# Kernel optimization log

Hardware: AMD Instinct MI355X
Metric: run time of the kernel (lower is better)

## Reference

```python
import jax, jax.numpy as jnp
import numpy as np

B, H, W = 2, 128, 128
MID = 64            # mid_channels
DG = 16             # deform_groups
MAX_RES = 10.0      # max_residue_magnitude
CIN_OFF = 3 * MID + 4   # 196: cat(extra_feat, flow_1, flow_2)
COFF = DG * 27          # 432: o1 + o2 + mask, each DG*9


def setup_inputs() -> dict:
    key = jax.random.key(0)
    ks = jax.random.split(key, 9)
    return {
        "extra_feat": jax.random.normal(ks[0], (B, 3 * MID, H, W), jnp.float32),
        "flow_1": jax.random.normal(ks[1], (B, 2, H, W), jnp.float32) * 2.0,
        "flow_2": jax.random.normal(ks[2], (B, 2, H, W), jnp.float32) * 2.0,
        "feat_prop": jax.random.normal(ks[3], (B, MID, H, W), jnp.float32),
        "feat_n2": jax.random.normal(ks[4], (B, MID, H, W), jnp.float32),
        "w_off": jax.random.normal(ks[5], (COFF, CIN_OFF, 3, 3), jnp.float32) * 0.02,
        "b_off": jax.random.normal(ks[6], (COFF,), jnp.float32) * 0.02,
        "dc_weight": jax.random.normal(ks[7], (MID, 2 * MID, 3, 3), jnp.float32) * 0.05,
        "dc_bias": jax.random.normal(ks[8], (MID,), jnp.float32) * 0.05,
    }


def _conv3x3(x, w, b):
    y = jax.lax.conv_general_dilated(
        x, w, window_strides=(1, 1), padding=((1, 1), (1, 1)),
        dimension_numbers=("NCHW", "OIHW", "NCHW"))
    return y + b[None, :, None, None]


def _deform_conv2d(inp, offset, mask, weight, bias):
    # inp: [B, Cin, H, W]; offset: [B, 2*DG*9, H, W] (per group, per kernel pos: (dy, dx));
    # mask: [B, DG*9, H, W]; weight: [Cout, Cin, 3, 3]; stride=1, pad=1, dil=1.
    Bb, Cin, Hi, Wi = inp.shape
    K = 9
    cg = Cin // DG
    Ho, Wo = Hi, Wi
    ki = jnp.repeat(jnp.arange(3), 3)  # kernel row index per flat k (row-major)
    kj = jnp.tile(jnp.arange(3), 3)
    base_y = (jnp.arange(Ho) - 1)[None, :, None] + ki[:, None, None]  # [K, Ho, 1]
    base_x = (jnp.arange(Wo) - 1)[None, None, :] + kj[:, None, None]  # [K, 1, Wo]
    off = offset.reshape(Bb, DG, K, 2, Ho, Wo)
    py = base_y[None, None] + off[:, :, :, 0]  # [B, DG, K, Ho, Wo]
    px = base_x[None, None] + off[:, :, :, 1]
    y0 = jnp.floor(py)
    x0 = jnp.floor(px)
    inp_g = inp.reshape(Bb, DG, cg, Hi * Wi)
    acc = jnp.zeros((Bb, DG, cg, K, Ho, Wo), inp.dtype)
    for dy in (0.0, 1.0):
        for dx in (0.0, 1.0):
            yc = y0 + dy
            xc = x0 + dx
            wgt = (1.0 - jnp.abs(py - yc)) * (1.0 - jnp.abs(px - xc))
            valid = (yc >= 0) & (yc < Hi) & (xc >= 0) & (xc < Wi)
            idx = (jnp.clip(yc, 0, Hi - 1) * Wi + jnp.clip(xc, 0, Wi - 1)).astype(jnp.int32)
            idx = jnp.broadcast_to(idx.reshape(Bb, DG, 1, K * Ho * Wo), (Bb, DG, cg, K * Ho * Wo))
            g = jnp.take_along_axis(inp_g, idx, axis=3).reshape(Bb, DG, cg, K, Ho, Wo)
            acc = acc + g * (wgt * valid)[:, :, None]
    sm = acc * mask.reshape(Bb, DG, 1, K, Ho, Wo)  # modulated samples
    wr = weight.reshape(weight.shape[0], DG, cg, K)
    out = jnp.einsum("bgckhw,ogck->bohw", sm, wr) + bias[None, :, None, None]
    return out


def reference(extra_feat, flow_1, flow_2, feat_prop, feat_n2, w_off, b_off, dc_weight, dc_bias):
    x = jnp.concatenate([extra_feat, flow_1, flow_2], axis=1)
    out = _conv3x3(x, w_off, b_off)
    o1, o2, m = jnp.split(out, 3, axis=1)  # each [B, DG*9, H, W]
    offset = MAX_RES * jnp.tanh(jnp.concatenate([o1, o2], axis=1))
    rep = DG * 3 * 3 // 2  # 72
    f1 = jnp.tile(flow_1[:, ::-1], (1, rep, 1, 1))  # flip(1): (dx,dy)->(dy,dx)
    f2 = jnp.tile(flow_2[:, ::-1], (1, rep, 1, 1))
    half = offset.shape[1] // 2
    offset = jnp.concatenate([offset[:, :half] + f1, offset[:, half:] + f2], axis=1)
    mask = jax.nn.sigmoid(m)
    inp = jnp.concatenate([feat_prop, feat_n2], axis=1)
    return _deform_conv2d(inp, offset, mask, dc_weight, dc_bias)
```

## Files before the change

### kernel.cpp

```cpp
#include <hip/hip_runtime.h>
#include <math.h>

#define Hh 128
#define Ww 128
#define HW (128*128)
#define CIN_OFF 196
#define COFF 432

typedef _Float16 half8 __attribute__((ext_vector_type(8)));
typedef _Float16 half4 __attribute__((ext_vector_type(4)));
typedef _Float16 half2v __attribute__((ext_vector_type(2)));
typedef float f32x4 __attribute__((ext_vector_type(4)));

static __device__ __forceinline__ half8 splat8(float v) {
  _Float16 h = (_Float16)v;
  half8 r = {h, h, h, h, h, h, h, h};
  return r;
}

__global__ __launch_bounds__(256) void k_prep_all(
    const float* __restrict__ dcw, const float* __restrict__ w_off,
    const float* __restrict__ fp, const float* __restrict__ fn2,
    _Float16* __restrict__ wH, _Float16* __restrict__ BpT, _Float16* __restrict__ Bt,
    _Float16* __restrict__ featT) {
  const int bid = blockIdx.x;
  if (bid < 3375) {
    const int idx = bid * 256 + (int)threadIdx.x;
    if (idx < 73728) {
      const int co = idx / 1152;
      const int j  = idx - co * 1152;
      const int k  = j >> 7;
      const int ci = j & 127;
      wH[idx] = (_Float16)dcw[(co * 128 + ci) * 9 + k];
    } else if (idx < 73728 + 774144) {
      const int j  = idx - 73728;
      const int c  = j & 7;
      const int n  = (j >> 3) % 448;
      const int sl = (j >> 3) / 448;
      const int l4 = sl & 3;
      const int s  = sl >> 2;
      const int t  = s / 6;
      const int cg = s - t * 6;
      const int ci = cg * 32 + l4 * 8 + c;
      BpT[j] = (_Float16)((n < COFF) ? w_off[((size_t)n * CIN_OFF + ci) * 9 + t] : 0.f);
    } else {
      const int j = idx - 73728 - 774144;
      const int c = j & 3;
      const int n = (j >> 2) % 448;
      const int t = (j >> 2) / 448;
      Bt[j] = (_Float16)((n < COFF) ? w_off[((size_t)n * CIN_OFF + 192 + c) * 9 + t] : 0.f);
    }
  } else {
    const int t = (bid - 3375) * 256 + (int)threadIdx.x;
    const int b = t >> 14;
    const int hw = t & 16383;
#pragma unroll
    for (int g = 0; g < 16; ++g) {
      const float* src = (g < 8) ? fp : fn2;
      const int ch0 = (g & 7) * 8;
      half8 v;
#pragma unroll
      for (int c = 0; c < 8; ++c)
        v[c] = (_Float16)src[(size_t)(b * 64 + ch0 + c) * HW + hw];
      *(half8*)(featT + (((size_t)(b * 16 + g)) * HW + hw) * 8) = v;
    }
  }
}

__global__ __launch_bounds__(512, 2) void k_offconv_mfma(
    const float* __restrict__ extra, const float* __restrict__ f1, const float* __restrict__ f2,
    const _Float16* __restrict__ BpT, const _Float16* __restrict__ Bt,
    const float* __restrict__ b_off,
    _Float16* __restrict__ off_pm, _Float16* __restrict__ mask_pm) {
  __shared__ __align__(16) _Float16 smA[3 * 130 * 192];
  __shared__ __align__(16) _Float16 smT[3 * 130 * 4];
  const int h    = blockIdx.x;
  const int b    = blockIdx.y;
  const int tid  = (int)threadIdx.x;
  const int lane = tid & 63;
  const int wid  = tid >> 6;
  const int wm   = wid & 1;
  const int wn   = (wid >> 1) & 3;
  const int m_base = wm * 64;
  const int n_base = wn * 112;
  const int l15 = lane & 15;
  const int l4  = lane >> 4;

  for (int z = tid; z < 588; z += 512) {
    const int p2 = z % 98;
    const int rr = z / 98;
    const int r  = (rr >= 3) ? (rr - 3) : rr;
    const int px = (rr >= 3) ? 129 : 0;
    if (p2 < 96) {
      const int ci = 2 * p2, biw = ci >> 3;
      const int sw = ((biw & 24) | ((biw & 7) ^ (px & 7))) << 3;
      *(half2v*)(smA + (r * 130 + px) * 192 + sw + (ci & 7)) = (half2v){(_Float16)0.f, (_Float16)0.f};
    } else {
      *(half2v*)(smT + (r * 130 + px) * 4 + 2 * (p2 - 96)) = (half2v){(_Float16)0.f, (_Float16)0.f};
    }
  }

#pragma unroll 3
  for (int j = 0; j < 18; ++j) {
    const int J   = tid + 512 * j;
    const int p2a = J & 15;
    const int qa  = (J >> 4) & 3;
    const int R   = J >> 6;
    const int r   = R / 48;
    const int rem = R - 48 * r;
    const int qh  = rem & 7;
    const int p2h = rem >> 3;
    const int q   = qa + 4 * qh;
    const int p2  = p2a + 16 * p2h;
    const int ci  = 2 * p2;
    const int gh  = h - 1 + r;
    float4 va = {0.f, 0.f, 0.f, 0.f}, vb = va;
    if ((unsigned)gh < (unsigned)Hh) {
      const float* xp = extra + (size_t)(b * 192 + ci) * HW + gh * Ww + 4 * q;
      va = *(const float4*)xp;
      vb = *(const float4*)(xp + HW);
    }
    const float av[4] = {va.x, va.y, va.z, va.w};
    const float bv[4] = {vb.x, vb.y, vb.z, vb.w};
    const int biw = p2 >> 2;
#pragma unroll
    for (int i = 0; i < 4; ++i) {
      const int px = 1 + 4 * q + i;
      const int sw = ((biw & 24) | ((biw & 7) ^ (px & 7))) << 3;
      half2v pk; pk[0] = (_Float16)av[i]; pk[1] = (_Float16)bv[i];
      *(half2v*)(smA + (r * 130 + px) * 192 + sw + (ci & 7)) = pk;
    }
  }
  if (tid < 192) {
    const int q   = tid & 31;
    const int p2t = (tid >> 5) & 1;
    const int r   = tid >> 6;
    const int gh  = h - 1 + r;
    float4 va = {0.f, 0.f, 0.f, 0.f}, vb = va;
    if ((unsigned)gh < (unsigned)Hh) {
      const float* xp = (p2t ? f2 : f1) + (size_t)(b * 2) * HW + gh * Ww + 4 * q;
      va = *(const float4*)xp;
      vb = *(const float4*)(xp + HW);
    }
    const float av[4] = {va.x, va.y, va.z, va.w};
    const float bv[4] = {vb.x, vb.y, vb.z, vb.w};
#pragma unroll
    for (int i = 0; i < 4; ++i) {
      const int px = 1 + 4 * q + i;
      half2v pk; pk[0] = (_Float16)av[i]; pk[1] = (_Float16)bv[i];
      *(half2v*)(smT + (r * 130 + px) * 4 + 2 * p2t) = pk;
    }
  }
  __syncthreads();

  f32x4 acc[4][7];
#pragma unroll
  for (int i = 0; i < 4; ++i)
#pragma unroll
    for (int j = 0; j < 7; ++j) acc[i][j] = (f32x4){0.f, 0.f, 0.f, 0.f};

  const bool lz = (l4 == 0);
#pragma unroll 3
  for (int t = 0; t < 9; ++t) {
    const int ki = t / 3;
    const int kj = t - 3 * ki;
#pragma unroll
    for (int cg = 0; cg < 6; ++cg) {
      const int s4 = ((t * 6 + cg) * 4 + l4) * 448;
      half8 bf[7];
#pragma unroll
      for (int f = 0; f < 7; ++f)
        bf[f] = *(const half8*)(BpT + (size_t)(s4 + n_base + f * 16 + l15) * 8);
      half8 af[4];
#pragma unroll
      for (int mf = 0; mf < 4; ++mf) {
        const int px = m_base + mf * 16 + l15 + kj;
        const int bi = cg * 4 + l4;
        af[mf] = *(const half8*)(smA + (ki * 130 + px) * 192 +
                                 (((bi & 24) | ((bi & 7) ^ (px & 7))) << 3));
      }
#pragma unroll
      for (int mf = 0; mf < 4; ++mf)
#pragma unroll
        for (int f = 0; f < 7; ++f)
          acc[mf][f] = __builtin_amdgcn_mfma_f32_16x16x32_f16(af[mf], bf[f], acc[mf][f], 0, 0, 0);
    }
    half8 aft[4];
#pragma unroll
    for (int mf = 0; mf < 4; ++mf) {
      const int px = m_base + mf * 16 + l15 + kj;
      const half4 tv = *(const half4*)(smT + (ki * 130 + px) * 4);
      half8 a = {0, 0, 0, 0, 0, 0, 0, 0};
      if (lz) { a[0] = tv[0]; a[1] = tv[1]; a[2] = tv[2]; a[3] = tv[3]; }
      aft[mf] = a;
    }
#pragma unroll
    for (int f = 0; f < 7; ++f) {
      const half4 wv = *(const half4*)(Bt + (size_t)(t * 448 + n_base + f * 16 + l15) * 4);
      half8 bb = {0, 0, 0, 0, 0, 0, 0, 0};
      if (lz) { bb[0] = wv[0]; bb[1] = wv[1]; bb[2] = wv[2]; bb[3] = wv[3]; }
#pragma unroll
      for (int mf = 0; mf < 4; ++mf)
        acc[mf][f] = __builtin_amdgcn_mfma_f32_16x16x32_f16(aft[mf], bb, acc[mf][f], 0, 0, 0);
    }
  }

  __syncthreads();
  _Float16* so = smA;
  const int hw0 = h * Ww;
#pragma unroll
  for (int f = 0; f < 7; ++f) {
    const int n = n_base + f * 16 + l15;
    const float bias = (n < COFF) ? b_off[n] : 0.f;
    const bool isOff = (n < 288);
    const float* fl = (n < 144) ? f1 : f2;
    const size_t fladd = (size_t)(b * 2 + ((n & 1) ^ 1)) * HW + hw0;
#pragma unroll
    for (int mf = 0; mf < 4; ++mf) {
#pragma unroll
      for (int rr = 0; rr < 4; ++rr) {
        const int px = m_base + mf * 16 + l4 * 4 + rr;
        const float v = acc[mf][f][rr] + bias;
        float val;
        if (isOff) {
          const float e = __expf(2.f * v);
          val = 10.f * (1.f - 2.f / (e + 1.f)) + fl[fladd + px];
        } else {
          val = 1.f / (1.f + __expf(-v));
        }
        so[px * 456 + n] = (_Float16)val;
      }
    }
  }
  __syncthreads();
  for (int T = tid; T < 4608; T += 512) {
    const int px = T / 36, c = T - px * 36;
    const half8 v = *(const half8*)(so + px * 456 + c * 8);
    *(half8*)(off_pm + ((size_t)b * HW + hw0 + px) * 288 + c * 8) = v;
  }
  for (int T = tid; T < 2304; T += 512) {
    const int px = T / 18, c = T - px * 18;
    const half8 v = *(const half8*)(so + px * 456 + 288 + c * 8);
    *(half8*)(mask_pm + ((size_t)b * HW + hw0 + px) * 144 + c * 8) = v;
  }
}

__global__ __launch_bounds__(256, 4) void k_deform2(
    const _Float16* __restrict__ featT, const _Float16* __restrict__ off_pm,
    const _Float16* __restrict__ mask_pm, const _Float16* __restrict__ wH,
    const float* __restrict__ dcb, float* __restrict__ out) {
  __shared__ __align__(16) char smem[16 * 1160 * 2];
  _Float16* sm = (_Float16*)smem;
  float* red = (float*)smem;
  const int w0  = blockIdx.x * 16;
  const int h   = blockIdx.y;
  const int b   = blockIdx.z;
  const int tid = (int)threadIdx.x;
  const int lane = tid & 63, wid = tid >> 6;
  const int l15 = lane & 15, l4 = lane >> 4;

  half2v offv[9];
  _Float16 mkv[9];
#pragma unroll
  for (int i = 0; i < 9; ++i) {
    const int p   = tid + i * 256;
    const int pix = p / 144;
    const int r   = p - pix * 144;
    const int w   = w0 + pix;
    const int hw  = h * Ww + w;
    offv[i] = *(const half2v*)(off_pm + ((size_t)b * HW + hw) * 288 + 2 * r);
    mkv[i]  = mask_pm[((size_t)b * HW + hw) * 144 + r];
  }
#pragma unroll
  for (int i = 0; i < 9; ++i) {
    const int p   = tid + i * 256;
    const int pix = p / 144;
    const int r   = p - pix * 144;
    const int g   = r / 9;
    const int k   = r - g * 9;
    const int w   = w0 + pix;
    const float mk = (float)mkv[i];
    const int ki = (k >= 6) ? 2 : (k >= 3 ? 1 : 0);
    const int kj = k - 3 * ki;
    const float py = (float)(h - 1 + ki) + (float)offv[i][0];
    const float px = (float)(w - 1 + kj) + (float)offv[i][1];
    const float y0f = floorf(py), x0f = floorf(px);
    const int y0 = (int)y0f, x0 = (int)x0f;
    const float ly = py - y0f, lx = px - x0f;
    const float hy = 1.f - ly, hx = 1.f - lx;
    const int y1 = y0 + 1, x1 = x0 + 1;
    const bool vy0 = (unsigned)y0 < (unsigned)Hh, vy1 = (unsigned)y1 < (unsigned)Hh;
    const bool vx0 = (unsigned)x0 < (unsigned)Ww, vx1 = (unsigned)x1 < (unsigned)Ww;
    const float w00 = (vy0 && vx0) ? hy * hx : 0.f;
    const float w01 = (vy0 && vx1) ? hy * lx : 0.f;
    const float w10 = (vy1 && vx0) ? ly * hx : 0.f;
    const float w11 = (vy1 && vx1) ? ly * lx : 0.f;
    const int cy0 = min(max(y0, 0), Hh - 1), cy1 = min(max(y1, 0), Hh - 1);
    const int cx0 = min(max(x0, 0), Ww - 1), cx1 = min(max(x1, 0), Ww - 1);
    const _Float16* gbase = featT + ((size_t)(b * 16 + g) * HW) * 8;
    const half8 s00 = *(const half8*)(gbase + (cy0 * Ww + cx0) * 8);
    const half8 s01 = *(const half8*)(gbase + (cy0 * Ww + cx1) * 8);
    const half8 s10 = *(const half8*)(gbase + (cy1 * Ww + cx0) * 8);
    const half8 s11 = *(const half8*)(gbase + (cy1 * Ww + cx1) * 8);
    half8 v = s00 * splat8(w00) + s01 * splat8(w01) + s10 * splat8(w10) + s11 * splat8(w11);
    v = v * splat8(mk);
    const int swz = (g ^ (k & 7)) << 3;
    *(half8*)(sm + pix * 1160 + k * 128 + swz) = v;
  }
  __syncthreads();

  f32x4 acc[4];
#pragma unroll
  for (int nf = 0; nf < 4; ++nf) acc[nf] = (f32x4){0.f, 0.f, 0.f, 0.f};
#pragma unroll
  for (int j = 0; j < 9; ++j) {
    const int s  = wid * 9 + j;
    const int k  = s >> 2;
    const int cg = s & 3;
    const int gidx = cg * 4 + l4;
    const half8 af = *(const half8*)(sm + l15 * 1160 + k * 128 + ((gidx ^ (k & 7)) << 3));
    const int koff = s * 32 + l4 * 8;
#pragma unroll
    for (int nf = 0; nf < 4; ++nf) {
      const half8 bf = *(const half8*)(wH + (nf * 16 + l15) * 1152 + koff);
      acc[nf] = __builtin_amdgcn_mfma_f32_16x16x32_f16(af, bf, acc[nf], 0, 0, 0);
    }
  }
  __syncthreads();
#pragma unroll
  for (int nf = 0; nf < 4; ++nf)
#pragma unroll
    for (int rr = 0; rr < 4; ++rr)
      red[(wid * 16 + l4 * 4 + rr) * 66 + nf * 16 + l15] = acc[nf][rr];
  __syncthreads();

  const int m  = tid & 15;
  const int ng = tid >> 4;
#pragma unroll
  for (int i = 0; i < 4; ++i) {
    const int n = ng + 16 * i;
    float val = red[(0 * 16 + m) * 66 + n] + red[(1 * 16 + m) * 66 + n] +
                red[(2 * 16 + m) * 66 + n] + red[(3 * 16 + m) * 66 + n];
    out[(size_t)(b * 64 + n) * HW + h * Ww + w0 + m] = val + dcb[n];
  }
}

extern "C" void kernel_launch(void* const* d_in, const int* in_sizes, int n_in,
                              void* d_out, int out_size, void* d_ws, size_t ws_size,
                              hipStream_t stream) {
  const float* extra = (const float*)d_in[0];
  const float* f1    = (const float*)d_in[1];
  const float* f2    = (const float*)d_in[2];
  const float* fp    = (const float*)d_in[3];
  const float* fn2   = (const float*)d_in[4];
  const float* w_off = (const float*)d_in[5];
  const float* b_off = (const float*)d_in[6];
  const float* dcw   = (const float*)d_in[7];
  const float* dcb   = (const float*)d_in[8];
  float* out = (float*)d_out;

  _Float16* off_pm  = (_Float16*)d_ws;
  _Float16* mask_pm = off_pm + (size_t)2 * 288 * HW;
  _Float16* featT   = mask_pm + (size_t)2 * 144 * HW;
  _Float16* BpT     = featT + (size_t)2 * 128 * HW;
  _Float16* Bt      = BpT + 774144;
  _Float16* wH      = Bt + 16128;

  hipLaunchKernelGGL(k_prep_all, dim3(3503), dim3(256), 0, stream,
                     dcw, w_off, fp, fn2, wH, BpT, Bt, featT);
  hipLaunchKernelGGL(k_offconv_mfma, dim3(128, 2), dim3(512), 0, stream,
                     extra, f1, f2, BpT, Bt, b_off, off_pm, mask_pm);
  hipLaunchKernelGGL(k_deform2, dim3(8, 128, 2), dim3(256), 0, stream,
                     featT, off_pm, mask_pm, wH, dcb, out);
}
```

Before: 185.1 us.

## Stage offset-conv weights through double-buffered LDS and split input channels into halves

The offset conv kernel no longer reads weight fragments straight from global memory inside the MFMA loop. It register-prefetches each weight slice and stores it into a double-buffered, XOR-swizzled LDS region, so the load overlaps the MFMA work of the previous slice. The input staging is split into two halves of 128 channels to fit the new LDS budget, and the flow channels are folded into the second half as an extra K slice, which removes the separate padded flow MFMA pass. In exchange the loop now has a block-wide barrier per slice, uses about 157 KB of LDS (one block per CU), and carries a larger, more padded weight buffer.

```diff
diff --git a/kernel.cpp b/kernel.cpp
--- a/kernel.cpp
+++ b/kernel.cpp
@@ -8,7 +8,6 @@
 #define COFF 432
 
 typedef _Float16 half8 __attribute__((ext_vector_type(8)));
-typedef _Float16 half4 __attribute__((ext_vector_type(4)));
 typedef _Float16 half2v __attribute__((ext_vector_type(2)));
 typedef float f32x4 __attribute__((ext_vector_type(4)));
 
@@ -21,10 +20,10 @@
 __global__ __launch_bounds__(256) void k_prep_all(
     const float* __restrict__ dcw, const float* __restrict__ w_off,
     const float* __restrict__ fp, const float* __restrict__ fn2,
-    _Float16* __restrict__ wH, _Float16* __restrict__ BpT, _Float16* __restrict__ Bt,
+    _Float16* __restrict__ wH, _Float16* __restrict__ BpT2,
     _Float16* __restrict__ featT) {
   const int bid = blockIdx.x;
-  if (bid < 3375) {
+  if (bid < 3816) {
     const int idx = bid * 256 + (int)threadIdx.x;
     if (idx < 73728) {
       const int co = idx / 1152;
@@ -32,26 +31,29 @@
       const int k  = j >> 7;
       const int ci = j & 127;
       wH[idx] = (_Float16)dcw[(co * 128 + ci) * 9 + k];
-    } else if (idx < 73728 + 774144) {
+    } else {
       const int j  = idx - 73728;
       const int c  = j & 7;
-      const int n  = (j >> 3) % 448;
+      const int m  = (j >> 3) % 448;
       const int sl = (j >> 3) / 448;
       const int l4 = sl & 3;
-      const int s  = sl >> 2;
-      const int t  = s / 6;
-      const int cg = s - t * 6;
-      const int ci = cg * 32 + l4 * 8 + c;
-      BpT[j] = (_Float16)((n < COFF) ? w_off[((size_t)n * CIN_OFF + ci) * 9 + t] : 0.f);
-    } else {
-      const int j = idx - 73728 - 774144;
-      const int c = j & 3;
-      const int n = (j >> 2) % 448;
-      const int t = (j >> 2) / 448;
-      Bt[j] = (_Float16)((n < COFF) ? w_off[((size_t)n * CIN_OFF + 192 + c) * 9 + t] : 0.f);
+      const int u  = sl >> 2;
+      const int t  = u / 7;
+      const int jj = u - t * 7;
+      const int n  = m ^ ((l4 & 1) << 2);
+      float v = 0.f;
+      if (n < COFF) {
+        if (jj < 6) {
+          const int ci = jj * 32 + l4 * 8 + c;
+          v = w_off[((size_t)n * CIN_OFF + ci) * 9 + t];
+        } else if (l4 == 0 && c < 4) {
+          v = w_off[((size_t)n * CIN_OFF + 192 + c) * 9 + t];
+        }
+      }
+      BpT2[j] = (_Float16)v;
     }
   } else {
-    const int t = (bid - 3375) * 256 + (int)threadIdx.x;
+    const int t = (bid - 3816) * 256 + (int)threadIdx.x;
     const int b = t >> 14;
     const int hw = t & 16383;
 #pragma unroll
@@ -69,11 +71,11 @@
 
 __global__ __launch_bounds__(512, 2) void k_offconv_mfma(
     const float* __restrict__ extra, const float* __restrict__ f1, const float* __restrict__ f2,
-    const _Float16* __restrict__ BpT, const _Float16* __restrict__ Bt,
-    const float* __restrict__ b_off,
+    const _Float16* __restrict__ BpT2, const float* __restrict__ b_off,
     _Float16* __restrict__ off_pm, _Float16* __restrict__ mask_pm) {
-  __shared__ __align__(16) _Float16 smA[3 * 130 * 192];
-  __shared__ __align__(16) _Float16 smT[3 * 130 * 4];
+  __shared__ __align__(16) char LDSBUF[157184];
+  _Float16* smA = (_Float16*)LDSBUF;
+  _Float16* smB = (_Float16*)(LDSBUF + 99840);
   const int h    = blockIdx.x;
   const int b    = blockIdx.y;
   const int tid  = (int)threadIdx.x;
@@ -85,71 +87,61 @@
   const int n_base = wn * 112;
   const int l15 = lane & 15;
   const int l4  = lane >> 4;
-
-  for (int z = tid; z < 588; z += 512) {
-    const int p2 = z % 98;
-    const int rr = z / 98;
-    const int r  = (rr >= 3) ? (rr - 3) : rr;
-    const int px = (rr >= 3) ? 129 : 0;
-    if (p2 < 96) {
-      const int ci = 2 * p2, biw = ci >> 3;
-      const int sw = ((biw & 24) | ((biw & 7) ^ (px & 7))) << 3;
-      *(half2v*)(smA + (r * 130 + px) * 192 + sw + (ci & 7)) = (half2v){(_Float16)0.f, (_Float16)0.f};
-    } else {
-      *(half2v*)(smT + (r * 130 + px) * 4 + 2 * (p2 - 96)) = (half2v){(_Float16)0.f, (_Float16)0.f};
-    }
-  }
-
-#pragma unroll 3
-  for (int j = 0; j < 18; ++j) {
-    const int J   = tid + 512 * j;
+  const int xr  = (l4 & 1) << 2;
+
+  if (tid < 384) {
+    const int pair = tid & 63;
+    const int rp   = tid >> 6;
+    const int r    = rp >> 1;
+    const int px   = (rp & 1) ? 129 : 0;
+    *(half2v*)(smA + (r * 130 + px) * 128 + pair * 2) =
+        (half2v){(_Float16)0.f, (_Float16)0.f};
+  }
+
+#pragma unroll 2
+  for (int it = 0; it < 12; ++it) {
+    const int J   = tid + 512 * it;
     const int p2a = J & 15;
     const int qa  = (J >> 4) & 3;
     const int R   = J >> 6;
-    const int r   = R / 48;
-    const int rem = R - 48 * r;
+    const int r   = R >> 5;
+    const int rem = R & 31;
     const int qh  = rem & 7;
     const int p2h = rem >> 3;
     const int q   = qa + 4 * qh;
     const int p2  = p2a + 16 * p2h;
-    const int ci  = 2 * p2;
+    const int cil = 2 * p2;
     const int gh  = h - 1 + r;
     float4 va = {0.f, 0.f, 0.f, 0.f}, vb = va;
     if ((unsigned)gh < (unsigned)Hh) {
-      const float* xp = extra + (size_t)(b * 192 + ci) * HW + gh * Ww + 4 * q;
+      const float* xp = extra + (size_t)(b * 192 + cil) * HW + gh * Ww + 4 * q;
       va = *(const float4*)xp;
       vb = *(const float4*)(xp + HW);
     }
     const float av[4] = {va.x, va.y, va.z, va.w};
     const float bv[4] = {vb.x, vb.y, vb.z, vb.w};
-    const int biw = p2 >> 2;
+    const int bi = p2 >> 2;
 #pragma unroll
     for (int i = 0; i < 4; ++i) {
       const int px = 1 + 4 * q + i;
-      const int sw = ((biw & 24) | ((biw & 7) ^ (px & 7))) << 3;
+      const int sw = (bi & 8) | ((bi & 7) ^ (px & 7));
       half2v pk; pk[0] = (_Float16)av[i]; pk[1] = (_Float16)bv[i];
-      *(half2v*)(smA + (r * 130 + px) * 192 + sw + (ci & 7)) = pk;
-    }
-  }
-  if (tid < 192) {
-    const int q   = tid & 31;
-    const int p2t = (tid >> 5) & 1;
-    const int r   = tid >> 6;
-    const int gh  = h - 1 + r;
-    float4 va = {0.f, 0.f, 0.f, 0.f}, vb = va;
-    if ((unsigned)gh < (unsigned)Hh) {
-      const float* xp = (p2t ? f2 : f1) + (size_t)(b * 2) * HW + gh * Ww + 4 * q;
-      va = *(const float4*)xp;
-      vb = *(const float4*)(xp + HW);
-    }
-    const float av[4] = {va.x, va.y, va.z, va.w};
-    const float bv[4] = {vb.x, vb.y, vb.z, vb.w};
-#pragma unroll
-    for (int i = 0; i < 4; ++i) {
-      const int px = 1 + 4 * q + i;
-      half2v pk; pk[0] = (_Float16)av[i]; pk[1] = (_Float16)bv[i];
-      *(half2v*)(smT + (r * 130 + px) * 4 + 2 * p2t) = pk;
-    }
+      *(half2v*)(smA + (r * 130 + px) * 128 + sw * 8 + (cil & 7)) = pk;
+    }
+  }
+
+  half8 breg0, breg1, breg2, breg3;
+  {
+    const _Float16* src = BpT2 + tid * 8;
+    breg0 = *(const half8*)src;
+    breg1 = *(const half8*)(src + 4096);
+    breg2 = *(const half8*)(src + 8192);
+    if (tid < 256) breg3 = *(const half8*)(src + 12288);
+    _Float16* dst = smB + tid * 8;
+    *(half8*)dst = breg0;
+    *(half8*)(dst + 4096) = breg1;
+    *(half8*)(dst + 8192) = breg2;
+    if (tid < 256) *(half8*)(dst + 12288) = breg3;
   }
   __syncthreads();
 
@@ -159,54 +151,98 @@
 #pragma unroll
     for (int j = 0; j < 7; ++j) acc[i][j] = (f32x4){0.f, 0.f, 0.f, 0.f};
 
-  const bool lz = (l4 == 0);
-#pragma unroll 3
-  for (int t = 0; t < 9; ++t) {
-    const int ki = t / 3;
-    const int kj = t - 3 * ki;
-#pragma unroll
-    for (int cg = 0; cg < 6; ++cg) {
-      const int s4 = ((t * 6 + cg) * 4 + l4) * 448;
-      half8 bf[7];
-#pragma unroll
-      for (int f = 0; f < 7; ++f)
-        bf[f] = *(const half8*)(BpT + (size_t)(s4 + n_base + f * 16 + l15) * 8);
-      half8 af[4];
-#pragma unroll
-      for (int mf = 0; mf < 4; ++mf) {
-        const int px = m_base + mf * 16 + l15 + kj;
-        const int bi = cg * 4 + l4;
-        af[mf] = *(const half8*)(smA + (ki * 130 + px) * 192 +
-                                 (((bi & 24) | ((bi & 7) ^ (px & 7))) << 3));
+  int u = 0;
+#pragma unroll 1
+  for (int hf = 0; hf < 2; ++hf) {
+    if (hf == 1) {
+#pragma unroll 2
+      for (int it = 0; it < 9; ++it) {
+        const int J   = tid + 512 * it;
+        const int p2a = J & 15;
+        const int qa  = (J >> 4) & 3;
+        const int R   = J >> 6;
+        const int r   = R / 24;
+        const int rem = R - 24 * r;
+        const int qh  = rem & 7;
+        const int p2h = rem >> 3;
+        const int q   = qa + 4 * qh;
+        const int p2  = p2a + 16 * p2h;
+        const int cil = 2 * p2;
+        const int gh  = h - 1 + r;
+        float4 va = {0.f, 0.f, 0.f, 0.f}, vb = va;
+        if ((unsigned)gh < (unsigned)Hh && p2 < 34) {
+          const float* xp;
+          if (p2 < 32)      xp = extra + (size_t)(b * 192 + 128 + cil) * HW;
+          else if (p2 == 32) xp = f1 + (size_t)(b * 2) * HW;
+          else               xp = f2 + (size_t)(b * 2) * HW;
+          va = *(const float4*)(xp + gh * Ww + 4 * q);
+          vb = *(const float4*)(xp + HW + gh * Ww + 4 * q);
+        }
+        const float av[4] = {va.x, va.y, va.z, va.w};
+        const float bv[4] = {vb.x, vb.y, vb.z, vb.w};
+        const int bi = p2 >> 2;
+#pragma unroll
+        for (int i = 0; i < 4; ++i) {
+          const int px = 1 + 4 * q + i;
+          const int sw = (bi & 8) | ((bi & 7) ^ (px & 7));
+          half2v pk; pk[0] = (_Float16)av[i]; pk[1] = (_Float16)bv[i];
+          *(half2v*)(smA + (r * 130 + px) * 128 + sw * 8 + (cil & 7)) = pk;
+        }
       }
-#pragma unroll
-      for (int mf = 0; mf < 4; ++mf)
-#pragma unroll
-        for (int f = 0; f < 7; ++f)
-          acc[mf][f] = __builtin_amdgcn_mfma_f32_16x16x32_f16(af[mf], bf[f], acc[mf][f], 0, 0, 0);
-    }
-    half8 aft[4];
-#pragma unroll
-    for (int mf = 0; mf < 4; ++mf) {
-      const int px = m_base + mf * 16 + l15 + kj;
-      const half4 tv = *(const half4*)(smT + (ki * 130 + px) * 4);
-      half8 a = {0, 0, 0, 0, 0, 0, 0, 0};
-      if (lz) { a[0] = tv[0]; a[1] = tv[1]; a[2] = tv[2]; a[3] = tv[3]; }
-      aft[mf] = a;
-    }
-#pragma unroll
-    for (int f = 0; f < 7; ++f) {
-      const half4 wv = *(const half4*)(Bt + (size_t)(t * 448 + n_base + f * 16 + l15) * 4);
-      half8 bb = {0, 0, 0, 0, 0, 0, 0, 0};
-      if (lz) { bb[0] = wv[0]; bb[1] = wv[1]; bb[2] = wv[2]; bb[3] = wv[3]; }
-#pragma unroll
-      for (int mf = 0; mf < 4; ++mf)
-        acc[mf][f] = __builtin_amdgcn_mfma_f32_16x16x32_f16(aft[mf], bb, acc[mf][f], 0, 0, 0);
-    }
-  }
-
-  __syncthreads();
-  _Float16* so = smA;
+      __syncthreads();
+    }
+    const int JL = hf ? 3 : 4;
+#pragma unroll 1
+    for (int t = 0; t < 9; ++t) {
+      const int ki = t / 3;
+      const int kj = t - 3 * ki;
+#pragma unroll 1
+      for (int jl = 0; jl < JL; ++jl) {
+        const int un = u + 1;
+        const bool pf = (un < 63);
+        if (pf) {
+          const int su = (un < 36) ? ((un >> 2) * 7 + (un & 3))
+                                   : (((un - 36) / 3) * 7 + 4 + (un - 36) % 3);
+          const _Float16* src = BpT2 + (size_t)su * 14336 + tid * 8;
+          breg0 = *(const half8*)src;
+          breg1 = *(const half8*)(src + 4096);
+          breg2 = *(const half8*)(src + 8192);
+          if (tid < 256) breg3 = *(const half8*)(src + 12288);
+        }
+        const _Float16* bb = smB + (u & 1) * 14336;
+        half8 bf[7];
+#pragma unroll
+        for (int f = 0; f < 7; ++f) {
+          const int nn = n_base + f * 16 + l15;
+          bf[f] = *(const half8*)(bb + (l4 * 448 + (nn ^ xr)) * 8);
+        }
+        const int bi = jl * 4 + l4;
+        half8 af[4];
+#pragma unroll
+        for (int mf = 0; mf < 4; ++mf) {
+          const int px = m_base + mf * 16 + l15 + kj;
+          af[mf] = *(const half8*)(smA + (ki * 130 + px) * 128 +
+                                   (((bi & 8) | ((bi & 7) ^ (px & 7))) << 3));
+        }
+#pragma unroll
+        for (int mf = 0; mf < 4; ++mf)
+#pragma unroll
+          for (int f = 0; f < 7; ++f)
+            acc[mf][f] = __builtin_amdgcn_mfma_f32_16x16x32_f16(af[mf], bf[f], acc[mf][f], 0, 0, 0);
+        if (pf) {
+          _Float16* dst = smB + (un & 1) * 14336 + tid * 8;
+          *(half8*)dst = breg0;
+          *(half8*)(dst + 4096) = breg1;
+          *(half8*)(dst + 8192) = breg2;
+          if (tid < 256) *(half8*)(dst + 12288) = breg3;
+        }
+        __syncthreads();
+        ++u;
+      }
+    }
+  }
+
+  _Float16* so = (_Float16*)LDSBUF;
   const int hw0 = h * Ww;
 #pragma unroll
   for (int f = 0; f < 7; ++f) {
@@ -362,14 +398,13 @@
   _Float16* off_pm  = (_Float16*)d_ws;
   _Float16* mask_pm = off_pm + (size_t)2 * 288 * HW;
   _Float16* featT   = mask_pm + (size_t)2 * 144 * HW;
-  _Float16* BpT     = featT + (size_t)2 * 128 * HW;
-  _Float16* Bt      = BpT + 774144;
-  _Float16* wH      = Bt + 16128;
-
-  hipLaunchKernelGGL(k_prep_all, dim3(3503), dim3(256), 0, stream,
-                     dcw, w_off, fp, fn2, wH, BpT, Bt, featT);
+  _Float16* BpT2    = featT + (size_t)2 * 128 * HW;
+  _Float16* wH      = BpT2 + 903168;
+
+  hipLaunchKernelGGL(k_prep_all, dim3(3944), dim3(256), 0, stream,
+                     dcw, w_off, fp, fn2, wH, BpT2, featT);
   hipLaunchKernelGGL(k_offconv_mfma, dim3(128, 2), dim3(512), 0, stream,
-                     extra, f1, f2, BpT, Bt, b_off, off_pm, mask_pm);
+                     extra, f1, f2, BpT2, b_off, off_pm, mask_pm);
   hipLaunchKernelGGL(k_deform2, dim3(8, 128, 2), dim3(256), 0, stream,
                      featT, off_pm, mask_pm, wH, dcb, out);
 }
```

Result: no change. 185.1 us (-0.0%).

## Split offset conv rows into two 64-column tiles for more blocks

Applied to the files above, without the earlier changes.

The offset-conv MFMA kernel now tiles each image row into two 64-pixel column tiles, launching twice as many blocks with halved LDS and accumulator footprint. Halo columns are loaded from neighboring pixels instead of zero padding. The aim is better CU occupancy and latency hiding. In exchange, each weight fragment read from global memory feeds only half as many MFMAs, and halo loading adds scalar reads.

```diff
diff --git a/kernel.cpp b/kernel.cpp
--- a/kernel.cpp
+++ b/kernel.cpp
@@ -67,56 +67,44 @@
   }
 }
 
-__global__ __launch_bounds__(512, 2) void k_offconv_mfma(
+__global__ __launch_bounds__(512, 4) void k_offconv_mfma(
     const float* __restrict__ extra, const float* __restrict__ f1, const float* __restrict__ f2,
     const _Float16* __restrict__ BpT, const _Float16* __restrict__ Bt,
     const float* __restrict__ b_off,
     _Float16* __restrict__ off_pm, _Float16* __restrict__ mask_pm) {
-  __shared__ __align__(16) _Float16 smA[3 * 130 * 192];
-  __shared__ __align__(16) _Float16 smT[3 * 130 * 4];
-  const int h    = blockIdx.x;
-  const int b    = blockIdx.y;
+  __shared__ __align__(16) _Float16 smA[3 * 66 * 192];
+  __shared__ __align__(16) _Float16 smT[3 * 66 * 4];
+  const int wt   = blockIdx.x;
+  const int h    = blockIdx.y;
+  const int b    = blockIdx.z;
+  const int w0   = wt * 64;
   const int tid  = (int)threadIdx.x;
   const int lane = tid & 63;
   const int wid  = tid >> 6;
   const int wm   = wid & 1;
   const int wn   = (wid >> 1) & 3;
-  const int m_base = wm * 64;
+  const int m_base = wm * 32;
   const int n_base = wn * 112;
   const int l15 = lane & 15;
   const int l4  = lane >> 4;
 
-  for (int z = tid; z < 588; z += 512) {
-    const int p2 = z % 98;
-    const int rr = z / 98;
-    const int r  = (rr >= 3) ? (rr - 3) : rr;
-    const int px = (rr >= 3) ? 129 : 0;
-    if (p2 < 96) {
-      const int ci = 2 * p2, biw = ci >> 3;
-      const int sw = ((biw & 24) | ((biw & 7) ^ (px & 7))) << 3;
-      *(half2v*)(smA + (r * 130 + px) * 192 + sw + (ci & 7)) = (half2v){(_Float16)0.f, (_Float16)0.f};
-    } else {
-      *(half2v*)(smT + (r * 130 + px) * 4 + 2 * (p2 - 96)) = (half2v){(_Float16)0.f, (_Float16)0.f};
-    }
-  }
-
 #pragma unroll 3
-  for (int j = 0; j < 18; ++j) {
-    const int J   = tid + 512 * j;
+  for (int it = 0; it < 9; ++it) {
+    const int J   = tid + 512 * it;
     const int p2a = J & 15;
     const int qa  = (J >> 4) & 3;
     const int R   = J >> 6;
-    const int r   = R / 48;
-    const int rem = R - 48 * r;
-    const int qh  = rem & 7;
-    const int p2h = rem >> 3;
+    const int r   = R / 24;
+    const int rem = R - 24 * r;
+    const int qh  = rem & 3;
+    const int p2h = rem >> 2;
     const int q   = qa + 4 * qh;
     const int p2  = p2a + 16 * p2h;
     const int ci  = 2 * p2;
     const int gh  = h - 1 + r;
     float4 va = {0.f, 0.f, 0.f, 0.f}, vb = va;
     if ((unsigned)gh < (unsigned)Hh) {
-      const float* xp = extra + (size_t)(b * 192 + ci) * HW + gh * Ww + 4 * q;
+      const float* xp = extra + (size_t)(b * 192 + ci) * HW + gh * Ww + w0 + 4 * q;
       va = *(const float4*)xp;
       vb = *(const float4*)(xp + HW);
     }
@@ -128,17 +116,18 @@
       const int px = 1 + 4 * q + i;
       const int sw = ((biw & 24) | ((biw & 7) ^ (px & 7))) << 3;
       half2v pk; pk[0] = (_Float16)av[i]; pk[1] = (_Float16)bv[i];
-      *(half2v*)(smA + (r * 130 + px) * 192 + sw + (ci & 7)) = pk;
-    }
-  }
-  if (tid < 192) {
-    const int q   = tid & 31;
-    const int p2t = (tid >> 5) & 1;
-    const int r   = tid >> 6;
+      *(half2v*)(smA + (r * 66 + px) * 192 + sw + (ci & 7)) = pk;
+    }
+  }
+  if (tid < 96) {
+    const int r   = tid >> 5;
+    const int rem = tid & 31;
+    const int pt  = rem >> 4;
+    const int q   = rem & 15;
     const int gh  = h - 1 + r;
     float4 va = {0.f, 0.f, 0.f, 0.f}, vb = va;
     if ((unsigned)gh < (unsigned)Hh) {
-      const float* xp = (p2t ? f2 : f1) + (size_t)(b * 2) * HW + gh * Ww + 4 * q;
+      const float* xp = (pt ? f2 : f1) + (size_t)(b * 2) * HW + gh * Ww + w0 + 4 * q;
       va = *(const float4*)xp;
       vb = *(const float4*)(xp + HW);
     }
@@ -148,14 +137,53 @@
     for (int i = 0; i < 4; ++i) {
       const int px = 1 + 4 * q + i;
       half2v pk; pk[0] = (_Float16)av[i]; pk[1] = (_Float16)bv[i];
-      *(half2v*)(smT + (r * 130 + px) * 4 + 2 * p2t) = pk;
-    }
-  }
-  __syncthreads();
-
-  f32x4 acc[4][7];
-#pragma unroll
-  for (int i = 0; i < 4; ++i)
+      *(half2v*)(smT + (r * 66 + px) * 4 + 2 * pt) = pk;
+    }
+  }
+  for (int z = tid; z < 588; z += 512) {
+    if (z < 576) {
+      const int r    = z / 192;
+      const int rem  = z - r * 192;
+      const int side = rem / 96;
+      const int p2   = rem - side * 96;
+      const int px   = side ? 65 : 0;
+      const int col  = w0 - 1 + px;
+      const int ci   = 2 * p2;
+      const int gh   = h - 1 + r;
+      float s0 = 0.f, s1 = 0.f;
+      if ((unsigned)gh < (unsigned)Hh && (unsigned)col < (unsigned)Ww) {
+        const float* xp = extra + (size_t)(b * 192 + ci) * HW + gh * Ww + col;
+        s0 = xp[0];
+        s1 = xp[HW];
+      }
+      const int biw = p2 >> 2;
+      const int sw = ((biw & 24) | ((biw & 7) ^ (px & 7))) << 3;
+      half2v pk; pk[0] = (_Float16)s0; pk[1] = (_Float16)s1;
+      *(half2v*)(smA + (r * 66 + px) * 192 + sw + (ci & 7)) = pk;
+    } else {
+      const int t2   = z - 576;
+      const int r    = t2 >> 2;
+      const int rem  = t2 & 3;
+      const int side = rem >> 1;
+      const int pt   = rem & 1;
+      const int px   = side ? 65 : 0;
+      const int col  = w0 - 1 + px;
+      const int gh   = h - 1 + r;
+      float s0 = 0.f, s1 = 0.f;
+      if ((unsigned)gh < (unsigned)Hh && (unsigned)col < (unsigned)Ww) {
+        const float* xp = (pt ? f2 : f1) + (size_t)(b * 2) * HW + gh * Ww + col;
+        s0 = xp[0];
+        s1 = xp[HW];
+      }
+      half2v pk; pk[0] = (_Float16)s0; pk[1] = (_Float16)s1;
+      *(half2v*)(smT + (r * 66 + px) * 4 + 2 * pt) = pk;
+    }
+  }
+  __syncthreads();
+
+  f32x4 acc[2][7];
+#pragma unroll
+  for (int i = 0; i < 2; ++i)
 #pragma unroll
     for (int j = 0; j < 7; ++j) acc[i][j] = (f32x4){0.f, 0.f, 0.f, 0.f};
 
@@ -171,25 +199,25 @@
 #pragma unroll
       for (int f = 0; f < 7; ++f)
         bf[f] = *(const half8*)(BpT + (size_t)(s4 + n_base + f * 16 + l15) * 8);
-      half8 af[4];
-#pragma unroll
-      for (int mf = 0; mf < 4; ++mf) {
+      half8 af[2];
+#pragma unroll
+      for (int mf = 0; mf < 2; ++mf) {
         const int px = m_base + mf * 16 + l15 + kj;
         const int bi = cg * 4 + l4;
-        af[mf] = *(const half8*)(smA + (ki * 130 + px) * 192 +
+        af[mf] = *(const half8*)(smA + (ki * 66 + px) * 192 +
                                  (((bi & 24) | ((bi & 7) ^ (px & 7))) << 3));
       }
 #pragma unroll
-      for (int mf = 0; mf < 4; ++mf)
+      for (int mf = 0; mf < 2; ++mf)
 #pragma unroll
         for (int f = 0; f < 7; ++f)
           acc[mf][f] = __builtin_amdgcn_mfma_f32_16x16x32_f16(af[mf], bf[f], acc[mf][f], 0, 0, 0);
     }
-    half8 aft[4];
-#pragma unroll
-    for (int mf = 0; mf < 4; ++mf) {
+    half8 aft[2];
+#pragma unroll
+    for (int mf = 0; mf < 2; ++mf) {
       const int px = m_base + mf * 16 + l15 + kj;
-      const half4 tv = *(const half4*)(smT + (ki * 130 + px) * 4);
+      const half4 tv = *(const half4*)(smT + (ki * 66 + px) * 4);
       half8 a = {0, 0, 0, 0, 0, 0, 0, 0};
       if (lz) { a[0] = tv[0]; a[1] = tv[1]; a[2] = tv[2]; a[3] = tv[3]; }
       aft[mf] = a;
@@ -200,14 +228,14 @@
       half8 bb = {0, 0, 0, 0, 0, 0, 0, 0};
       if (lz) { bb[0] = wv[0]; bb[1] = wv[1]; bb[2] = wv[2]; bb[3] = wv[3]; }
 #pragma unroll
-      for (int mf = 0; mf < 4; ++mf)
+      for (int mf = 0; mf < 2; ++mf)
         acc[mf][f] = __builtin_amdgcn_mfma_f32_16x16x32_f16(aft[mf], bb, acc[mf][f], 0, 0, 0);
     }
   }
 
   __syncthreads();
   _Float16* so = smA;
-  const int hw0 = h * Ww;
+  const int hw0 = h * Ww + w0;
 #pragma unroll
   for (int f = 0; f < 7; ++f) {
     const int n = n_base + f * 16 + l15;
@@ -216,7 +244,7 @@
     const float* fl = (n < 144) ? f1 : f2;
     const size_t fladd = (size_t)(b * 2 + ((n & 1) ^ 1)) * HW + hw0;
 #pragma unroll
-    for (int mf = 0; mf < 4; ++mf) {
+    for (int mf = 0; mf < 2; ++mf) {
 #pragma unroll
       for (int rr = 0; rr < 4; ++rr) {
         const int px = m_base + mf * 16 + l4 * 4 + rr;
@@ -233,12 +261,12 @@
     }
   }
   __syncthreads();
-  for (int T = tid; T < 4608; T += 512) {
+  for (int T = tid; T < 2304; T += 512) {
     const int px = T / 36, c = T - px * 36;
     const half8 v = *(const half8*)(so + px * 456 + c * 8);
     *(half8*)(off_pm + ((size_t)b * HW + hw0 + px) * 288 + c * 8) = v;
   }
-  for (int T = tid; T < 2304; T += 512) {
+  for (int T = tid; T < 1152; T += 512) {
     const int px = T / 18, c = T - px * 18;
     const half8 v = *(const half8*)(so + px * 456 + 288 + c * 8);
     *(half8*)(mask_pm + ((size_t)b * HW + hw0 + px) * 144 + c * 8) = v;
@@ -368,7 +396,7 @@
 
   hipLaunchKernelGGL(k_prep_all, dim3(3503), dim3(256), 0, stream,
                      dcw, w_off, fp, fn2, wH, BpT, Bt, featT);
-  hipLaunchKernelGGL(k_offconv_mfma, dim3(128, 2), dim3(512), 0, stream,
+  hipLaunchKernelGGL(k_offconv_mfma, dim3(2, 128, 2), dim3(512), 0, stream,
                      extra, f1, f2, BpT, Bt, b_off, off_pm, mask_pm);
   hipLaunchKernelGGL(k_deform2, dim3(8, 128, 2), dim3(256), 0, stream,
                      featT, off_pm, mask_pm, wH, dcb, out);
```

Result: no change. 186.2 us (+0.6%).

## Widen deform tile to 32 pixels and restructure offset-weight prep loop

Applied to the files above, without the earlier changes.

The deform kernel now processes 32 output pixels per 512-thread block. Waves split across two 16-pixel halves and four K-quarters, so each wH B-fragment load serves twice as many pixels. Separately, the prep kernel's offset-conv weight repack now has each thread read 9 contiguous taps for one (n, ci) pair. This replaces a per-element scatter with scattered reads and cuts the prep grid from 3503 to 815 blocks. The trade-offs are doubled LDS per block, fewer blocks in the deform grid, and strided stores in the repack.

```diff
diff --git a/kernel.cpp b/kernel.cpp
--- a/kernel.cpp
+++ b/kernel.cpp
@@ -24,34 +24,36 @@
     _Float16* __restrict__ wH, _Float16* __restrict__ BpT, _Float16* __restrict__ Bt,
     _Float16* __restrict__ featT) {
   const int bid = blockIdx.x;
-  if (bid < 3375) {
+  if (bid < 288) {
     const int idx = bid * 256 + (int)threadIdx.x;
-    if (idx < 73728) {
-      const int co = idx / 1152;
-      const int j  = idx - co * 1152;
-      const int k  = j >> 7;
-      const int ci = j & 127;
-      wH[idx] = (_Float16)dcw[(co * 128 + ci) * 9 + k];
-    } else if (idx < 73728 + 774144) {
-      const int j  = idx - 73728;
-      const int c  = j & 7;
-      const int n  = (j >> 3) % 448;
-      const int sl = (j >> 3) / 448;
-      const int l4 = sl & 3;
-      const int s  = sl >> 2;
-      const int t  = s / 6;
-      const int cg = s - t * 6;
-      const int ci = cg * 32 + l4 * 8 + c;
-      BpT[j] = (_Float16)((n < COFF) ? w_off[((size_t)n * CIN_OFF + ci) * 9 + t] : 0.f);
-    } else {
-      const int j = idx - 73728 - 774144;
+    const int co = idx / 1152;
+    const int j  = idx - co * 1152;
+    const int k  = j >> 7;
+    const int ci = j & 127;
+    wH[idx] = (_Float16)dcw[(co * 128 + ci) * 9 + k];
+  } else if (bid < 624) {
+    const int idx = (bid - 288) * 256 + (int)threadIdx.x;
+    const int n  = idx / 192;
+    const int ci = idx - n * 192;
+    const int l4 = (ci >> 3) & 3;
+    const int c  = ci & 7;
+    const int cg = ci >> 5;
+    const float* src = w_off + ((size_t)n * CIN_OFF + ci) * 9;
+#pragma unroll
+    for (int t = 0; t < 9; ++t) {
+      const float v = (n < COFF) ? src[t] : 0.f;
+      BpT[((size_t)((t * 6 + cg) * 4 + l4) * 448 + n) * 8 + c] = (_Float16)v;
+    }
+  } else if (bid < 687) {
+    const int j = (bid - 624) * 256 + (int)threadIdx.x;
+    if (j < 16128) {
       const int c = j & 3;
       const int n = (j >> 2) % 448;
       const int t = (j >> 2) / 448;
       Bt[j] = (_Float16)((n < COFF) ? w_off[((size_t)n * CIN_OFF + 192 + c) * 9 + t] : 0.f);
     }
   } else {
-    const int t = (bid - 3375) * 256 + (int)threadIdx.x;
+    const int t = (bid - 687) * 256 + (int)threadIdx.x;
     const int b = t >> 14;
     const int hw = t & 16383;
 #pragma unroll
@@ -245,14 +247,14 @@
   }
 }
 
-__global__ __launch_bounds__(256, 4) void k_deform2(
+__global__ __launch_bounds__(512, 2) void k_deform2(
     const _Float16* __restrict__ featT, const _Float16* __restrict__ off_pm,
     const _Float16* __restrict__ mask_pm, const _Float16* __restrict__ wH,
     const float* __restrict__ dcb, float* __restrict__ out) {
-  __shared__ __align__(16) char smem[16 * 1160 * 2];
+  __shared__ __align__(16) char smem[32 * 1160 * 2];
   _Float16* sm = (_Float16*)smem;
   float* red = (float*)smem;
-  const int w0  = blockIdx.x * 16;
+  const int w0  = blockIdx.x * 32;
   const int h   = blockIdx.y;
   const int b   = blockIdx.z;
   const int tid = (int)threadIdx.x;
@@ -263,7 +265,7 @@
   _Float16 mkv[9];
 #pragma unroll
   for (int i = 0; i < 9; ++i) {
-    const int p   = tid + i * 256;
+    const int p   = tid + i * 512;
     const int pix = p / 144;
     const int r   = p - pix * 144;
     const int w   = w0 + pix;
@@ -273,7 +275,7 @@
   }
 #pragma unroll
   for (int i = 0; i < 9; ++i) {
-    const int p   = tid + i * 256;
+    const int p   = tid + i * 512;
     const int pix = p / 144;
     const int r   = p - pix * 144;
     const int g   = r / 9;
@@ -309,16 +311,19 @@
   }
   __syncthreads();
 
+  const int mh = wid & 1;
+  const int kq = wid >> 1;
   f32x4 acc[4];
 #pragma unroll
   for (int nf = 0; nf < 4; ++nf) acc[nf] = (f32x4){0.f, 0.f, 0.f, 0.f};
 #pragma unroll
   for (int j = 0; j < 9; ++j) {
-    const int s  = wid * 9 + j;
+    const int s  = kq * 9 + j;
     const int k  = s >> 2;
     const int cg = s & 3;
     const int gidx = cg * 4 + l4;
-    const half8 af = *(const half8*)(sm + l15 * 1160 + k * 128 + ((gidx ^ (k & 7)) << 3));
+    const half8 af = *(const half8*)(sm + (mh * 16 + l15) * 1160 + k * 128 +
+                                     ((gidx ^ (k & 7)) << 3));
     const int koff = s * 32 + l4 * 8;
 #pragma unroll
     for (int nf = 0; nf < 4; ++nf) {
@@ -331,17 +336,19 @@
   for (int nf = 0; nf < 4; ++nf)
 #pragma unroll
     for (int rr = 0; rr < 4; ++rr)
-      red[(wid * 16 + l4 * 4 + rr) * 66 + nf * 16 + l15] = acc[nf][rr];
-  __syncthreads();
-
-  const int m  = tid & 15;
-  const int ng = tid >> 4;
-#pragma unroll
-  for (int i = 0; i < 4; ++i) {
-    const int n = ng + 16 * i;
-    float val = red[(0 * 16 + m) * 66 + n] + red[(1 * 16 + m) * 66 + n] +
-                red[(2 * 16 + m) * 66 + n] + red[(3 * 16 + m) * 66 + n];
-    out[(size_t)(b * 64 + n) * HW + h * Ww + w0 + m] = val + dcb[n];
+      red[((mh * 4 + kq) * 16 + l4 * 4 + rr) * 66 + nf * 16 + l15] = acc[nf][rr];
+  __syncthreads();
+
+  for (int T = tid; T < 2048; T += 512) {
+    const int px2 = T & 31;
+    const int n   = T >> 5;
+    const int mhr = px2 >> 4;
+    const int pxl = px2 & 15;
+    float val = red[((mhr * 4 + 0) * 16 + pxl) * 66 + n] +
+                red[((mhr * 4 + 1) * 16 + pxl) * 66 + n] +
+                red[((mhr * 4 + 2) * 16 + pxl) * 66 + n] +
+                red[((mhr * 4 + 3) * 16 + pxl) * 66 + n];
+    out[(size_t)(b * 64 + n) * HW + h * Ww + w0 + px2] = val + dcb[n];
   }
 }
 
@@ -366,10 +373,10 @@
   _Float16* Bt      = BpT + 774144;
   _Float16* wH      = Bt + 16128;
 
-  hipLaunchKernelGGL(k_prep_all, dim3(3503), dim3(256), 0, stream,
+  hipLaunchKernelGGL(k_prep_all, dim3(815), dim3(256), 0, stream,
                      dcw, w_off, fp, fn2, wH, BpT, Bt, featT);
   hipLaunchKernelGGL(k_offconv_mfma, dim3(128, 2), dim3(512), 0, stream,
                      extra, f1, f2, BpT, Bt, b_off, off_pm, mask_pm);
-  hipLaunchKernelGGL(k_deform2, dim3(8, 128, 2), dim3(256), 0, stream,
+  hipLaunchKernelGGL(k_deform2, dim3(4, 128, 2), dim3(512), 0, stream,
                      featT, off_pm, mask_pm, wH, dcb, out);
 }
```

Result: faster. 176.7 us (-4.5%).
